# Performance work log

Hardware: AMD Instinct MI355X
Metric: run time of the kernel (lower is better)

Reference implementation:

```python
import jax, jax.numpy as jnp
import numpy as np

# Module config (mirrors SWTLayer(__init__) with dimensions=[64,64,16], kmax=[3,3], wavelet='db1')
DIMS = (64, 64)      # spatial sizes along axes 1,2
LEVELS = (6, 6)      # pywt.dwt_max_level(64, dec_len=2) == 6 (Haar)
KMAX = (3, 3)
NLIFT = 16
BATCH = 32


def swt_haar(x, level, axis):
    """pywt.swt(x, 'db1', level, trim_approx=True, norm=True) along `axis` (periodic).
    norm=True Haar level-j step s=2^(j-1): cA[i]=(a[i]+a[i+s])/2, cD[i]=(a[i]-a[i+s])/2.
    Returns concat([cA_n, cD_n, ..., cD_1]) along axis (length (level+1)*M)."""
    a = x
    details = []
    for j in range(level):
        s = 2 ** j
        sh = jnp.roll(a, -s, axis)   # a[i + s] (periodic)
        details.append((a - sh) * 0.5)
        a = (a + sh) * 0.5
    return jnp.concatenate([a] + details[::-1], axis=axis)


def iswt_haar(xt, level, axis):
    """pywt.iswt inverse of swt_haar: averages the two phase reconstructions per level."""
    bands = jnp.split(xt, level + 1, axis=axis)  # [cA_n, cD_n, ..., cD_1]
    a = bands[0]
    for j in range(level, 0, -1):
        cD = bands[level - j + 1]
        s = 2 ** (j - 1)
        a = 0.5 * ((a + cD) + jnp.roll(a - cD, s, axis))
    return a


def setup_inputs() -> dict:
    key = jax.random.key(0)
    k1, k2, k3 = jax.random.split(key, 3)
    x = jax.random.normal(k1, (BATCH, DIMS[0], DIMS[1], NLIFT), dtype=jnp.float32)
    W = jax.random.uniform(
        k2,
        (NLIFT, NLIFT, DIMS[0] * (LEVELS[0] + 1), DIMS[1] * (LEVELS[1] + 1)),
        dtype=jnp.float32,
    )
    b = jax.random.normal(k3, (NLIFT, NLIFT), dtype=jnp.float32)
    return {"x": x, "weights": W, "bias": b}


def reference(x, weights, bias):
    # forward SWT along each spatial axis -> (B, 448, 448, C)
    xt = x
    for i, L in enumerate(LEVELS):
        xt = swt_haar(xt, L, axis=i + 1)
    # truncate: zero wavenumber bands [kmax*M, level*M) along each spatial axis
    for i, (M, L, K) in enumerate(zip(DIMS, LEVELS, KMAX)):
        idx = (slice(None),) * (i + 1) + (slice(K * M, L * M),)
        xt = xt.at[idx].set(0.0)
    # per-location channel mixing: 'abcd,debc->abce'
    xt = jnp.einsum('abcd,debc->abce', xt, weights)
    # inverse SWT back to (B, 64, 64, C)
    out = xt
    for i, L in enumerate(LEVELS):
        out = iswt_haar(out, L, axis=i + 1)
    # skip path: F.linear(x, bias) == x @ bias.T
    return out + x @ bias.T
```

## Files before the change

### kernel.cpp

```cpp
#include <hip/hip_runtime.h>
#include <cstddef>
#include <cstdint>


#define X1_IDX(a,u,j,d) ((((size_t)(a)*256 + (u))*64 + (j))*16 + (d))

__global__ __launch_bounds__(256, 2) void k_swt1(const float* __restrict__ x,
                                                 float* __restrict__ X1) {
  __shared__ float col[64 * 64];
  __shared__ float Ps[4][64];
  const int t = threadIdx.x;
  const int q = t >> 6, c = t & 63, jl = c >> 4, d = c & 15;
  const int a = blockIdx.x, j = blockIdx.y * 4 + jl;
  const float* xp = x + ((size_t)a * 4096 + j) * 16 + d + (size_t)(q * 16) * 1024;
  float P = 0.f;
#pragma unroll
  for (int r = 0; r < 16; ++r) {
    float v = xp[(size_t)r * 1024];
    col[(q * 16 + r) * 64 + c] = v;
    P += v;
  }
  Ps[q][c] = P;
  __syncthreads();
  const float cA = (Ps[0][c] + Ps[1][c] + Ps[2][c] + Ps[3][c]) * 0.015625f;
  float w4 = Ps[q][c], w4b = Ps[(q + 1) & 3][c];
  float w5 = w4 + w4b;
  float* X1p = X1 + X1_IDX(a, 0, j, d);
#pragma unroll
  for (int r = 0; r < 16; ++r) {
    const int u = q * 16 + r;
    const float c0 = col[u * 64 + c];
    const float c1 = col[((u + 1) & 63) * 64 + c];
    const float c16 = col[((u + 16) & 63) * 64 + c];
    const float c32 = col[((u + 32) & 63) * 64 + c];
    X1p[(size_t)(u) * 1024]       = cA;
    X1p[(size_t)(64 + u) * 1024]  = w5 * 0.03125f - cA;
    X1p[(size_t)(128 + u) * 1024] = (w4 - w4b) * 0.03125f;
    X1p[(size_t)(192 + u) * 1024] = (c0 - c1) * 0.5f;
    w4 += c16 - c0;
    w4b += c32 - c16;
    w5 += c32 - c0;
  }
}

#define TSS 20
#define TSA (256 * TSS)
#define TS2(a,v,d) ((a) * TSA + (v) * TSS + (d))
#define WLS 18

__global__ __launch_bounds__(256, 2) void k_fused(float* __restrict__ X1,
                                                  const float* __restrict__ W) {
  __shared__ float Ts[2 * TSA];
  __shared__ float Wl[2 * 256 * WLS];
  __shared__ float Ps[2 * 8 * 16];
  const int t = threadIdx.x;
  const int bid = blockIdx.x;
  const int u = (bid & 7) + 8 * (bid >> 7);
  const int ac = (bid >> 3) & 15;
  const int a0 = ac * 2;
  const int ub = u >> 6;
  const int Brow = (ub == 3 ? 6 : ub) * 64 + (u & 63);

  const int aA = t >> 7, qA = (t >> 4) & 7, dA = t & 15;

  {
    const float* xp = X1 + X1_IDX(a0 + aA, u, qA * 8, dA);
    float P = 0.f;
#pragma unroll
    for (int r = 0; r < 8; ++r) {
      float v = xp[r * 16];
      Ts[TS2(aA, 192 + qA * 8 + r, dA)] = v;
      P += v;
    }
    Ps[aA * 128 + qA * 16 + dA] = P;
  }
  __syncthreads();
  {
    float cA = 0.f;
#pragma unroll
    for (int k = 0; k < 8; ++k) cA += Ps[aA * 128 + k * 16 + dA];
    cA *= 0.015625f;
    float w4 = Ps[aA * 128 + qA * 16 + dA] + Ps[aA * 128 + (((qA + 1) & 7) * 16) + dA];
    float w4b = Ps[aA * 128 + (((qA + 2) & 7) * 16) + dA] + Ps[aA * 128 + (((qA + 3) & 7) * 16) + dA];
    float w5 = w4 + w4b;
    float cd1[8];
#pragma unroll
    for (int r = 0; r < 8; ++r) {
      const int v = qA * 8 + r;
      const float c0 = Ts[TS2(aA, 192 + v, dA)];
      const float c1 = Ts[TS2(aA, 192 + ((v + 1) & 63), dA)];
      const float c16 = Ts[TS2(aA, 192 + ((v + 16) & 63), dA)];
      const float c32 = Ts[TS2(aA, 192 + ((v + 32) & 63), dA)];
      Ts[TS2(aA, v, dA)]       = cA;
      Ts[TS2(aA, 64 + v, dA)]  = w5 * 0.03125f - cA;
      Ts[TS2(aA, 128 + v, dA)] = (w4 - w4b) * 0.03125f;
      cd1[r] = (c0 - c1) * 0.5f;
      w4 += c16 - c0;
      w4b += c32 - c16;
      w5 += c32 - c0;
    }
    __syncthreads();
#pragma unroll
    for (int r = 0; r < 8; ++r) Ts[TS2(aA, 192 + qA * 8 + r, dA)] = cd1[r];
  }
  __syncthreads();

  const int vl = t >> 4, e = t & 15;
  const float* wbase = W + (size_t)t * 200704 + (size_t)Brow * 448;
  float4 pw0, pw1, pw2, pw3;
  {
    const float* wp = wbase;
    pw0 = *(const float4*)(wp + 0);
    pw1 = *(const float4*)(wp + 4);
    pw2 = *(const float4*)(wp + 8);
    pw3 = *(const float4*)(wp + 12);
  }
  for (int vg = 0; vg < 16; ++vg) {
    const int buf = vg & 1;
    {
      float* wrow = &Wl[(buf * 256 + t) * WLS];
      *(float2*)&wrow[0]  = make_float2(pw0.x, pw0.y);
      *(float2*)&wrow[2]  = make_float2(pw0.z, pw0.w);
      *(float2*)&wrow[4]  = make_float2(pw1.x, pw1.y);
      *(float2*)&wrow[6]  = make_float2(pw1.z, pw1.w);
      *(float2*)&wrow[8]  = make_float2(pw2.x, pw2.y);
      *(float2*)&wrow[10] = make_float2(pw2.z, pw2.w);
      *(float2*)&wrow[12] = make_float2(pw3.x, pw3.y);
      *(float2*)&wrow[14] = make_float2(pw3.z, pw3.w);
    }
    __syncthreads();
    if (vg < 15) {
      const int v2 = vg + 1;
      const int kb2 = v2 >> 2;
      const float* wp = wbase + (kb2 == 3 ? 384 : kb2 * 64) + (v2 & 3) * 16;
      pw0 = *(const float4*)(wp + 0);
      pw1 = *(const float4*)(wp + 4);
      pw2 = *(const float4*)(wp + 8);
      pw3 = *(const float4*)(wp + 12);
    }
    float wreg[16];
#pragma unroll
    for (int d = 0; d < 16; ++d)
      wreg[d] = Wl[(buf * 256 + d * 16 + e) * WLS + vl];
    const int v = vg * 16 + vl;
#pragma unroll
    for (int a = 0; a < 2; ++a) {
      const float4 t0 = *(const float4*)&Ts[TS2(a, v, 0)];
      const float4 t1 = *(const float4*)&Ts[TS2(a, v, 4)];
      const float4 t2 = *(const float4*)&Ts[TS2(a, v, 8)];
      const float4 t3 = *(const float4*)&Ts[TS2(a, v, 12)];
      float acc = t0.x * wreg[0] + t0.y * wreg[1] + t0.z * wreg[2] + t0.w * wreg[3]
                + t1.x * wreg[4] + t1.y * wreg[5] + t1.z * wreg[6] + t1.w * wreg[7]
                + t2.x * wreg[8] + t2.y * wreg[9] + t2.z * wreg[10] + t2.w * wreg[11]
                + t3.x * wreg[12] + t3.y * wreg[13] + t3.z * wreg[14] + t3.w * wreg[15];
      Ts[TS2(a, v, e)] = acc;
    }
  }
  __syncthreads();

  {
    const int aC = t >> 7, qC = (t >> 4) & 7, eC = t & 15;
    float rg[8];
#pragma unroll
    for (int r = 0; r < 8; ++r) {
      const int i = qC * 8 + r, i2 = (i - 32) & 63;
      rg[r] = 0.5f * (Ts[TS2(aC, i, eC)] + Ts[TS2(aC, 64 + i, eC)]
                    + Ts[TS2(aC, i2, eC)] - Ts[TS2(aC, 64 + i2, eC)]);
    }
    __syncthreads();
#pragma unroll
    for (int r = 0; r < 8; ++r) Ts[TS2(aC, qC * 8 + r, eC)] = rg[r];
    __syncthreads();
#pragma unroll
    for (int r = 0; r < 8; ++r) {
      const int i = qC * 8 + r, i2 = (i - 16) & 63;
      rg[r] = 0.5f * (Ts[TS2(aC, i, eC)] + Ts[TS2(aC, 128 + i, eC)]
                    + Ts[TS2(aC, i2, eC)] - Ts[TS2(aC, 128 + i2, eC)]);
    }
    __syncthreads();
#pragma unroll
    for (int r = 0; r < 8; ++r) Ts[TS2(aC, 64 + qC * 8 + r, eC)] = rg[r];
    __syncthreads();
#pragma unroll
    for (int r = 0; r < 8; ++r) {
      const int i = qC * 8 + r;
      float s = 0.f;
#pragma unroll
      for (int k = 0; k < 8; ++k) s += Ts[TS2(aC, 64 + ((i - 2 * k) & 63), eC)];
      rg[r] = s * 0.125f;
    }
    __syncthreads();
#pragma unroll
    for (int r = 0; r < 8; ++r) Ts[TS2(aC, qC * 8 + r, eC)] = rg[r];
    __syncthreads();
    float* zp = X1 + X1_IDX(a0 + aC, u, 0, eC);
#pragma unroll
    for (int r = 0; r < 8; ++r) {
      const int i = qC * 8 + r, i2 = (i - 1) & 63;
      zp[i * 16] = 0.5f * (Ts[TS2(aC, i, eC)] + Ts[TS2(aC, 192 + i, eC)]
                         + Ts[TS2(aC, i2, eC)] - Ts[TS2(aC, 192 + i2, eC)]);
    }
  }
}

__global__ __launch_bounds__(256, 2) void k_iswt1(const float* __restrict__ Z1,
                                                  const float* __restrict__ x,
                                                  const float* __restrict__ bias,
                                                  float* __restrict__ out) {
  __shared__ float A[64 * 64], Bb[64 * 64], D[64 * 64], xs[64 * 64];
  const int t = threadIdx.x;
  const int q = t >> 6, c = t & 63, jl = c >> 4, e = c & 15;
  const int a = blockIdx.x, j = blockIdx.y * 4 + jl;
  float breg[16];
  {
    const float4 b0 = *(const float4*)&bias[e * 16 + 0];
    const float4 b1 = *(const float4*)&bias[e * 16 + 4];
    const float4 b2 = *(const float4*)&bias[e * 16 + 8];
    const float4 b3 = *(const float4*)&bias[e * 16 + 12];
    breg[0]=b0.x; breg[1]=b0.y; breg[2]=b0.z; breg[3]=b0.w;
    breg[4]=b1.x; breg[5]=b1.y; breg[6]=b1.z; breg[7]=b1.w;
    breg[8]=b2.x; breg[9]=b2.y; breg[10]=b2.z; breg[11]=b2.w;
    breg[12]=b3.x; breg[13]=b3.y; breg[14]=b3.z; breg[15]=b3.w;
  }
  const float* Zp = Z1 + (size_t)a * 262144 + (size_t)j * 16 + e;
#pragma unroll
  for (int r = 0; r < 16; ++r) {
    const int i = q * 16 + r;
    A[i * 64 + c] = Zp[(size_t)i * 1024];
    D[i * 64 + c] = Zp[(size_t)(64 + i) * 1024];
    xs[i * 64 + c] = x[((size_t)a * 4096 + (size_t)i * 64 + j) * 16 + e];
  }
  __syncthreads();
  float rg[16];
#pragma unroll
  for (int r = 0; r < 16; ++r) {
    const int i = q * 16 + r, i2 = (i - 32) & 63;
    rg[r] = 0.5f * (A[i * 64 + c] + D[i * 64 + c] + A[i2 * 64 + c] - D[i2 * 64 + c]);
  }
  __syncthreads();
#pragma unroll
  for (int r = 0; r < 16; ++r) {
    const int i = q * 16 + r;
    Bb[i * 64 + c] = rg[r];
    D[i * 64 + c] = Zp[(size_t)(128 + i) * 1024];
  }
  __syncthreads();
#pragma unroll
  for (int r = 0; r < 16; ++r) {
    const int i = q * 16 + r, i2 = (i - 16) & 63;
    rg[r] = 0.5f * (Bb[i * 64 + c] + D[i * 64 + c] + Bb[i2 * 64 + c] - D[i2 * 64 + c]);
  }
  __syncthreads();
#pragma unroll
  for (int r = 0; r < 16; ++r) {
    const int i = q * 16 + r;
    A[i * 64 + c] = rg[r];
    D[i * 64 + c] = Zp[(size_t)(192 + i) * 1024];
  }
  __syncthreads();
#pragma unroll
  for (int r = 0; r < 16; ++r) {
    const int i = q * 16 + r;
    float s = 0.f;
#pragma unroll
    for (int k = 0; k < 8; ++k) s += A[((i - 2 * k) & 63) * 64 + c];
    rg[r] = s * 0.125f;
  }
  __syncthreads();
#pragma unroll
  for (int r = 0; r < 16; ++r) Bb[(q * 16 + r) * 64 + c] = rg[r];
  __syncthreads();
#pragma unroll
  for (int r = 0; r < 16; ++r) {
    const int i = q * 16 + r, i2 = (i - 1) & 63;
    float v = 0.5f * (Bb[i * 64 + c] + D[i * 64 + c] + Bb[i2 * 64 + c] - D[i2 * 64 + c]);
    float s = 0.f;
#pragma unroll
    for (int dd = 0; dd < 16; ++dd) s += xs[i * 64 + jl * 16 + dd] * breg[dd];
    out[((size_t)a * 4096 + (size_t)i * 64 + j) * 16 + e] = v + s;
  }
}

extern "C" void kernel_launch(void* const* d_in, const int* in_sizes, int n_in,
                              void* d_out, int out_size, void* d_ws, size_t ws_size,
                              hipStream_t stream) {
  const float* x = (const float*)d_in[0];
  const float* W = (const float*)d_in[1];
  const float* bias = (const float*)d_in[2];
  float* out = (float*)d_out;
  float* X1 = (float*)d_ws;

  k_swt1<<<dim3(32, 16), 256, 0, stream>>>(x, X1);
  k_fused<<<dim3(4096), 256, 0, stream>>>(X1, W);
  k_iswt1<<<dim3(32, 16), 256, 0, stream>>>(X1, x, bias, out);
}
```

Measured before the change: 421.0 us.

## Batch eight samples per fused block with dedicated weight-loader threads and register tiling

The fused kernel now handles 8 batch samples per block (512 threads, 1024 blocks), so each weight tile fetched from global memory is reused across 8 samples instead of 2. One wavefront acts as a dedicated weight loader that prefetches the next tile while 128 compute threads each calculate a 4x4 sample-by-output-channel register tile. The forward SWT kernel is vectorized to float4 over channels, the 8-tap running sum in both inverse stages becomes a sliding-window update, and the bias skip path uses float4 shared loads. Only a quarter of the threads do the einsum, and the larger shared footprint limits occupancy, which may cost latency hiding.

```diff
diff --git a/kernel.cpp b/kernel.cpp
--- a/kernel.cpp
+++ b/kernel.cpp
@@ -7,198 +7,264 @@
 
 __global__ __launch_bounds__(256, 2) void k_swt1(const float* __restrict__ x,
                                                  float* __restrict__ X1) {
-  __shared__ float col[64 * 64];
-  __shared__ float Ps[4][64];
+  __shared__ float col[64 * 256];
+  __shared__ float Ps[4 * 256];
   const int t = threadIdx.x;
-  const int q = t >> 6, c = t & 63, jl = c >> 4, d = c & 15;
-  const int a = blockIdx.x, j = blockIdx.y * 4 + jl;
-  const float* xp = x + ((size_t)a * 4096 + j) * 16 + d + (size_t)(q * 16) * 1024;
-  float P = 0.f;
-#pragma unroll
-  for (int r = 0; r < 16; ++r) {
-    float v = xp[(size_t)r * 1024];
-    col[(q * 16 + r) * 64 + c] = v;
-    P += v;
-  }
-  Ps[q][c] = P;
-  __syncthreads();
-  const float cA = (Ps[0][c] + Ps[1][c] + Ps[2][c] + Ps[3][c]) * 0.015625f;
-  float w4 = Ps[q][c], w4b = Ps[(q + 1) & 3][c];
-  float w5 = w4 + w4b;
-  float* X1p = X1 + X1_IDX(a, 0, j, d);
+  const int q = t >> 6;
+  const int cc = (t & 63) * 4;
+  const int jl = (t & 63) >> 2, dq = t & 3;
+  const int a = blockIdx.x, j = blockIdx.y * 16 + jl;
+  const float4* xp4 = (const float4*)(x + ((size_t)a * 4096 + j) * 16 + dq * 4);
+  float4 P = make_float4(0.f, 0.f, 0.f, 0.f);
+#pragma unroll
+  for (int r = 0; r < 16; ++r) {
+    const int i = q * 16 + r;
+    float4 v = xp4[(size_t)i * 256];
+    *(float4*)&col[i * 256 + cc] = v;
+    P.x += v.x; P.y += v.y; P.z += v.z; P.w += v.w;
+  }
+  *(float4*)&Ps[q * 256 + cc] = P;
+  __syncthreads();
+  const float4 p0 = *(const float4*)&Ps[0 * 256 + cc];
+  const float4 p1 = *(const float4*)&Ps[1 * 256 + cc];
+  const float4 p2 = *(const float4*)&Ps[2 * 256 + cc];
+  const float4 p3 = *(const float4*)&Ps[3 * 256 + cc];
+  float4 cA;
+  cA.x = (p0.x + p1.x + p2.x + p3.x) * 0.015625f;
+  cA.y = (p0.y + p1.y + p2.y + p3.y) * 0.015625f;
+  cA.z = (p0.z + p1.z + p2.z + p3.z) * 0.015625f;
+  cA.w = (p0.w + p1.w + p2.w + p3.w) * 0.015625f;
+  float4 w4 = *(const float4*)&Ps[q * 256 + cc];
+  float4 w4b = *(const float4*)&Ps[((q + 1) & 3) * 256 + cc];
+  float4 w5;
+  w5.x = w4.x + w4b.x; w5.y = w4.y + w4b.y; w5.z = w4.z + w4b.z; w5.w = w4.w + w4b.w;
+  float4* X1p = (float4*)(X1 + X1_IDX(a, 0, j, dq * 4));
+  float4 c0 = *(const float4*)&col[(q * 16) * 256 + cc];
 #pragma unroll
   for (int r = 0; r < 16; ++r) {
     const int u = q * 16 + r;
-    const float c0 = col[u * 64 + c];
-    const float c1 = col[((u + 1) & 63) * 64 + c];
-    const float c16 = col[((u + 16) & 63) * 64 + c];
-    const float c32 = col[((u + 32) & 63) * 64 + c];
-    X1p[(size_t)(u) * 1024]       = cA;
-    X1p[(size_t)(64 + u) * 1024]  = w5 * 0.03125f - cA;
-    X1p[(size_t)(128 + u) * 1024] = (w4 - w4b) * 0.03125f;
-    X1p[(size_t)(192 + u) * 1024] = (c0 - c1) * 0.5f;
-    w4 += c16 - c0;
-    w4b += c32 - c16;
-    w5 += c32 - c0;
+    const float4 c1 = *(const float4*)&col[((u + 1) & 63) * 256 + cc];
+    const float4 c16 = *(const float4*)&col[((u + 16) & 63) * 256 + cc];
+    const float4 c32 = *(const float4*)&col[((u + 32) & 63) * 256 + cc];
+    float4 b1, b2v, b3;
+    b1.x = w5.x * 0.03125f - cA.x; b1.y = w5.y * 0.03125f - cA.y;
+    b1.z = w5.z * 0.03125f - cA.z; b1.w = w5.w * 0.03125f - cA.w;
+    b2v.x = (w4.x - w4b.x) * 0.03125f; b2v.y = (w4.y - w4b.y) * 0.03125f;
+    b2v.z = (w4.z - w4b.z) * 0.03125f; b2v.w = (w4.w - w4b.w) * 0.03125f;
+    b3.x = (c0.x - c1.x) * 0.5f; b3.y = (c0.y - c1.y) * 0.5f;
+    b3.z = (c0.z - c1.z) * 0.5f; b3.w = (c0.w - c1.w) * 0.5f;
+    X1p[(size_t)u * 256] = cA;
+    X1p[(size_t)(64 + u) * 256] = b1;
+    X1p[(size_t)(128 + u) * 256] = b2v;
+    X1p[(size_t)(192 + u) * 256] = b3;
+    w4.x += c16.x - c0.x; w4.y += c16.y - c0.y; w4.z += c16.z - c0.z; w4.w += c16.w - c0.w;
+    w4b.x += c32.x - c16.x; w4b.y += c32.y - c16.y; w4b.z += c32.z - c16.z; w4b.w += c32.w - c16.w;
+    w5.x += c32.x - c0.x; w5.y += c32.y - c0.y; w5.z += c32.z - c0.z; w5.w += c32.w - c0.w;
+    c0 = c1;
   }
 }
 
-#define TSS 20
-#define TSA (256 * TSS)
-#define TS2(a,v,d) ((a) * TSA + (v) * TSS + (d))
-#define WLS 18
-
-__global__ __launch_bounds__(256, 2) void k_fused(float* __restrict__ X1,
+#define TSA 4104
+#define TS(a,v,d) ((a) * TSA + (v) * 16 + (d))
+#define WLS_E 324
+#define WLS_V 20
+
+__global__ __launch_bounds__(512, 1) void k_fused(float* __restrict__ X1,
                                                   const float* __restrict__ W) {
-  __shared__ float Ts[2 * TSA];
-  __shared__ float Wl[2 * 256 * WLS];
-  __shared__ float Ps[2 * 8 * 16];
+  __shared__ float Ts[8 * TSA];
+  __shared__ float Wl[16 * WLS_E];
+  __shared__ float Ps[8 * 4 * 16];
   const int t = threadIdx.x;
   const int bid = blockIdx.x;
-  const int u = (bid & 7) + 8 * (bid >> 7);
-  const int ac = (bid >> 3) & 15;
-  const int a0 = ac * 2;
+  const int u = (bid & 7) * 32 + (bid >> 5);
+  const int ac = (bid >> 3) & 3;
+  const int a0 = ac * 8;
   const int ub = u >> 6;
   const int Brow = (ub == 3 ? 6 : ub) * 64 + (u & 63);
 
-  const int aA = t >> 7, qA = (t >> 4) & 7, dA = t & 15;
+  const bool isLoader = (t >= 128 && t < 192);
+  const int ldq = (t >> 4) & 3, lel = t & 15;
+  float pw[4][16];
+
+  if (isLoader) {
+#pragma unroll
+    for (int jd = 0; jd < 4; ++jd) {
+      const int d = ldq * 4 + jd;
+      const float* wp = W + (size_t)(d * 16 + lel) * 200704 + (size_t)Brow * 448;
+#pragma unroll
+      for (int vq = 0; vq < 4; ++vq) {
+        float4 v = *(const float4*)(wp + vq * 4);
+        pw[jd][vq * 4 + 0] = v.x; pw[jd][vq * 4 + 1] = v.y;
+        pw[jd][vq * 4 + 2] = v.z; pw[jd][vq * 4 + 3] = v.w;
+      }
+    }
+  }
 
   {
-    const float* xp = X1 + X1_IDX(a0 + aA, u, qA * 8, dA);
+    const int aA = t >> 6, qA = (t >> 4) & 3, dA = t & 15;
+    const float* xpA = X1 + X1_IDX(a0 + aA, u, qA * 16, dA);
     float P = 0.f;
 #pragma unroll
-    for (int r = 0; r < 8; ++r) {
-      float v = xp[r * 16];
-      Ts[TS2(aA, 192 + qA * 8 + r, dA)] = v;
+    for (int r = 0; r < 16; ++r) {
+      float v = xpA[r * 16];
+      Ts[TS(aA, 192 + qA * 16 + r, dA)] = v;
       P += v;
     }
-    Ps[aA * 128 + qA * 16 + dA] = P;
-  }
-  __syncthreads();
+    Ps[(aA * 4 + qA) * 16 + dA] = P;
+    __syncthreads();
+    const float S = Ps[(aA * 4 + 0) * 16 + dA] + Ps[(aA * 4 + 1) * 16 + dA]
+                  + Ps[(aA * 4 + 2) * 16 + dA] + Ps[(aA * 4 + 3) * 16 + dA];
+    const float cA = S * 0.015625f;
+    float w4 = Ps[(aA * 4 + qA) * 16 + dA];
+    float w4b = Ps[(aA * 4 + ((qA + 1) & 3)) * 16 + dA];
+    float w5 = w4 + w4b;
+    float cd1[16];
+    float c0 = Ts[TS(aA, 192 + qA * 16, dA)];
+#pragma unroll
+    for (int r = 0; r < 16; ++r) {
+      const int v = qA * 16 + r;
+      const float c1 = Ts[TS(aA, 192 + ((v + 1) & 63), dA)];
+      const float c16 = Ts[TS(aA, 192 + ((v + 16) & 63), dA)];
+      const float c32 = Ts[TS(aA, 192 + ((v + 32) & 63), dA)];
+      Ts[TS(aA, v, dA)] = cA;
+      Ts[TS(aA, 64 + v, dA)] = w5 * 0.03125f - cA;
+      Ts[TS(aA, 128 + v, dA)] = (w4 - w4b) * 0.03125f;
+      cd1[r] = (c0 - c1) * 0.5f;
+      w4 += c16 - c0; w4b += c32 - c16; w5 += c32 - c0;
+      c0 = c1;
+    }
+    __syncthreads();
+#pragma unroll
+    for (int r = 0; r < 16; ++r) Ts[TS(aA, 192 + qA * 16 + r, dA)] = cd1[r];
+  }
+  __syncthreads();
+  if (isLoader) {
+#pragma unroll
+    for (int vl = 0; vl < 16; ++vl) {
+      float4 o = make_float4(pw[0][vl], pw[1][vl], pw[2][vl], pw[3][vl]);
+      *(float4*)&Wl[lel * WLS_E + vl * WLS_V + ldq * 4] = o;
+    }
+  }
+  __syncthreads();
+
   {
-    float cA = 0.f;
-#pragma unroll
-    for (int k = 0; k < 8; ++k) cA += Ps[aA * 128 + k * 16 + dA];
-    cA *= 0.015625f;
-    float w4 = Ps[aA * 128 + qA * 16 + dA] + Ps[aA * 128 + (((qA + 1) & 7) * 16) + dA];
-    float w4b = Ps[aA * 128 + (((qA + 2) & 7) * 16) + dA] + Ps[aA * 128 + (((qA + 3) & 7) * 16) + dA];
-    float w5 = w4 + w4b;
-    float cd1[8];
-#pragma unroll
-    for (int r = 0; r < 8; ++r) {
-      const int v = qA * 8 + r;
-      const float c0 = Ts[TS2(aA, 192 + v, dA)];
-      const float c1 = Ts[TS2(aA, 192 + ((v + 1) & 63), dA)];
-      const float c16 = Ts[TS2(aA, 192 + ((v + 16) & 63), dA)];
-      const float c32 = Ts[TS2(aA, 192 + ((v + 32) & 63), dA)];
-      Ts[TS2(aA, v, dA)]       = cA;
-      Ts[TS2(aA, 64 + v, dA)]  = w5 * 0.03125f - cA;
-      Ts[TS2(aA, 128 + v, dA)] = (w4 - w4b) * 0.03125f;
-      cd1[r] = (c0 - c1) * 0.5f;
-      w4 += c16 - c0;
-      w4b += c32 - c16;
-      w5 += c32 - c0;
-    }
-    __syncthreads();
-#pragma unroll
-    for (int r = 0; r < 8; ++r) Ts[TS2(aA, 192 + qA * 8 + r, dA)] = cd1[r];
-  }
-  __syncthreads();
-
-  const int vl = t >> 4, e = t & 15;
-  const float* wbase = W + (size_t)t * 200704 + (size_t)Brow * 448;
-  float4 pw0, pw1, pw2, pw3;
+    const bool isCompute = (t < 128);
+    const int at = t >> 6, et = (t >> 4) & 3, vlB = t & 15;
+    for (int vg = 0; vg < 16; ++vg) {
+      float4 tf[4][4], wf[4][4];
+      float acc[4][4];
+      if (isCompute) {
+        const int v = vg * 16 + vlB;
+#pragma unroll
+        for (int ja = 0; ja < 4; ++ja)
+#pragma unroll
+          for (int dq = 0; dq < 4; ++dq)
+            tf[ja][dq] = *(const float4*)&Ts[TS(at * 4 + ja, v, dq * 4)];
+#pragma unroll
+        for (int je = 0; je < 4; ++je)
+#pragma unroll
+          for (int dq = 0; dq < 4; ++dq)
+            wf[je][dq] = *(const float4*)&Wl[(et * 4 + je) * WLS_E + vlB * WLS_V + dq * 4];
+      }
+      if (isLoader && vg < 15) {
+        const int v2 = vg + 1, kb = v2 >> 2;
+        const int Ccol = (kb == 3 ? 6 : kb) * 64 + (v2 & 3) * 16;
+#pragma unroll
+        for (int jd = 0; jd < 4; ++jd) {
+          const int d = ldq * 4 + jd;
+          const float* wp = W + (size_t)(d * 16 + lel) * 200704 + (size_t)Brow * 448 + Ccol;
+#pragma unroll
+          for (int vq = 0; vq < 4; ++vq) {
+            float4 v = *(const float4*)(wp + vq * 4);
+            pw[jd][vq * 4 + 0] = v.x; pw[jd][vq * 4 + 1] = v.y;
+            pw[jd][vq * 4 + 2] = v.z; pw[jd][vq * 4 + 3] = v.w;
+          }
+        }
+      }
+      if (isCompute) {
+#pragma unroll
+        for (int ja = 0; ja < 4; ++ja)
+#pragma unroll
+          for (int je = 0; je < 4; ++je) {
+            float s = 0.f;
+#pragma unroll
+            for (int dq = 0; dq < 4; ++dq) {
+              s += tf[ja][dq].x * wf[je][dq].x;
+              s += tf[ja][dq].y * wf[je][dq].y;
+              s += tf[ja][dq].z * wf[je][dq].z;
+              s += tf[ja][dq].w * wf[je][dq].w;
+            }
+            acc[ja][je] = s;
+          }
+      }
+      __syncthreads();
+      if (isCompute) {
+        const int v = vg * 16 + vlB;
+#pragma unroll
+        for (int ja = 0; ja < 4; ++ja) {
+          float4 o = make_float4(acc[ja][0], acc[ja][1], acc[ja][2], acc[ja][3]);
+          *(float4*)&Ts[TS(at * 4 + ja, v, et * 4)] = o;
+        }
+      }
+      if (isLoader && vg < 15) {
+#pragma unroll
+        for (int vl = 0; vl < 16; ++vl) {
+          float4 o = make_float4(pw[0][vl], pw[1][vl], pw[2][vl], pw[3][vl]);
+          *(float4*)&Wl[lel * WLS_E + vl * WLS_V + ldq * 4] = o;
+        }
+      }
+      __syncthreads();
+    }
+  }
+
   {
-    const float* wp = wbase;
-    pw0 = *(const float4*)(wp + 0);
-    pw1 = *(const float4*)(wp + 4);
-    pw2 = *(const float4*)(wp + 8);
-    pw3 = *(const float4*)(wp + 12);
-  }
-  for (int vg = 0; vg < 16; ++vg) {
-    const int buf = vg & 1;
+    const int aC = t >> 6, qC = (t >> 4) & 3, eC = t & 15;
+    float rg[16];
+#pragma unroll
+    for (int r = 0; r < 16; ++r) {
+      const int i = qC * 16 + r, i2 = (i - 32) & 63;
+      rg[r] = 0.5f * (Ts[TS(aC, i, eC)] + Ts[TS(aC, 64 + i, eC)]
+                    + Ts[TS(aC, i2, eC)] - Ts[TS(aC, 64 + i2, eC)]);
+    }
+    __syncthreads();
+#pragma unroll
+    for (int r = 0; r < 16; ++r) Ts[TS(aC, qC * 16 + r, eC)] = rg[r];
+    __syncthreads();
+#pragma unroll
+    for (int r = 0; r < 16; ++r) {
+      const int i = qC * 16 + r, i2 = (i - 16) & 63;
+      rg[r] = 0.5f * (Ts[TS(aC, i, eC)] + Ts[TS(aC, 128 + i, eC)]
+                    + Ts[TS(aC, i2, eC)] - Ts[TS(aC, 128 + i2, eC)]);
+    }
+    __syncthreads();
+#pragma unroll
+    for (int r = 0; r < 16; ++r) Ts[TS(aC, 64 + qC * 16 + r, eC)] = rg[r];
+    __syncthreads();
     {
-      float* wrow = &Wl[(buf * 256 + t) * WLS];
-      *(float2*)&wrow[0]  = make_float2(pw0.x, pw0.y);
-      *(float2*)&wrow[2]  = make_float2(pw0.z, pw0.w);
-      *(float2*)&wrow[4]  = make_float2(pw1.x, pw1.y);
-      *(float2*)&wrow[6]  = make_float2(pw1.z, pw1.w);
-      *(float2*)&wrow[8]  = make_float2(pw2.x, pw2.y);
-      *(float2*)&wrow[10] = make_float2(pw2.z, pw2.w);
-      *(float2*)&wrow[12] = make_float2(pw3.x, pw3.y);
-      *(float2*)&wrow[14] = make_float2(pw3.z, pw3.w);
-    }
-    __syncthreads();
-    if (vg < 15) {
-      const int v2 = vg + 1;
-      const int kb2 = v2 >> 2;
-      const float* wp = wbase + (kb2 == 3 ? 384 : kb2 * 64) + (v2 & 3) * 16;
-      pw0 = *(const float4*)(wp + 0);
-      pw1 = *(const float4*)(wp + 4);
-      pw2 = *(const float4*)(wp + 8);
-      pw3 = *(const float4*)(wp + 12);
-    }
-    float wreg[16];
-#pragma unroll
-    for (int d = 0; d < 16; ++d)
-      wreg[d] = Wl[(buf * 256 + d * 16 + e) * WLS + vl];
-    const int v = vg * 16 + vl;
-#pragma unroll
-    for (int a = 0; a < 2; ++a) {
-      const float4 t0 = *(const float4*)&Ts[TS2(a, v, 0)];
-      const float4 t1 = *(const float4*)&Ts[TS2(a, v, 4)];
-      const float4 t2 = *(const float4*)&Ts[TS2(a, v, 8)];
-      const float4 t3 = *(const float4*)&Ts[TS2(a, v, 12)];
-      float acc = t0.x * wreg[0] + t0.y * wreg[1] + t0.z * wreg[2] + t0.w * wreg[3]
-                + t1.x * wreg[4] + t1.y * wreg[5] + t1.z * wreg[6] + t1.w * wreg[7]
-                + t2.x * wreg[8] + t2.y * wreg[9] + t2.z * wreg[10] + t2.w * wreg[11]
-                + t3.x * wreg[12] + t3.y * wreg[13] + t3.z * wreg[14] + t3.w * wreg[15];
-      Ts[TS2(a, v, e)] = acc;
-    }
-  }
-  __syncthreads();
-
-  {
-    const int aC = t >> 7, qC = (t >> 4) & 7, eC = t & 15;
-    float rg[8];
-#pragma unroll
-    for (int r = 0; r < 8; ++r) {
-      const int i = qC * 8 + r, i2 = (i - 32) & 63;
-      rg[r] = 0.5f * (Ts[TS2(aC, i, eC)] + Ts[TS2(aC, 64 + i, eC)]
-                    + Ts[TS2(aC, i2, eC)] - Ts[TS2(aC, 64 + i2, eC)]);
-    }
-    __syncthreads();
-#pragma unroll
-    for (int r = 0; r < 8; ++r) Ts[TS2(aC, qC * 8 + r, eC)] = rg[r];
-    __syncthreads();
-#pragma unroll
-    for (int r = 0; r < 8; ++r) {
-      const int i = qC * 8 + r, i2 = (i - 16) & 63;
-      rg[r] = 0.5f * (Ts[TS2(aC, i, eC)] + Ts[TS2(aC, 128 + i, eC)]
-                    + Ts[TS2(aC, i2, eC)] - Ts[TS2(aC, 128 + i2, eC)]);
-    }
-    __syncthreads();
-#pragma unroll
-    for (int r = 0; r < 8; ++r) Ts[TS2(aC, 64 + qC * 8 + r, eC)] = rg[r];
-    __syncthreads();
-#pragma unroll
-    for (int r = 0; r < 8; ++r) {
-      const int i = qC * 8 + r;
-      float s = 0.f;
-#pragma unroll
-      for (int k = 0; k < 8; ++k) s += Ts[TS2(aC, 64 + ((i - 2 * k) & 63), eC)];
-      rg[r] = s * 0.125f;
-    }
-    __syncthreads();
-#pragma unroll
-    for (int r = 0; r < 8; ++r) Ts[TS2(aC, qC * 8 + r, eC)] = rg[r];
+      float s0 = 0.f, s1 = 0.f;
+#pragma unroll
+      for (int k = 0; k < 8; ++k) s0 += Ts[TS(aC, 64 + ((qC * 16 - 2 * k) & 63), eC)];
+#pragma unroll
+      for (int k = 0; k < 8; ++k) s1 += Ts[TS(aC, 64 + ((qC * 16 + 1 - 2 * k) & 63), eC)];
+      rg[0] = s0 * 0.125f; rg[1] = s1 * 0.125f;
+#pragma unroll
+      for (int r = 2; r < 16; ++r) {
+        const int i = qC * 16 + r;
+        const float add = Ts[TS(aC, 64 + i, eC)] - Ts[TS(aC, 64 + ((i - 16) & 63), eC)];
+        if (r & 1) { s1 += add; rg[r] = s1 * 0.125f; }
+        else       { s0 += add; rg[r] = s0 * 0.125f; }
+      }
+    }
+    __syncthreads();
+#pragma unroll
+    for (int r = 0; r < 16; ++r) Ts[TS(aC, qC * 16 + r, eC)] = rg[r];
     __syncthreads();
     float* zp = X1 + X1_IDX(a0 + aC, u, 0, eC);
 #pragma unroll
-    for (int r = 0; r < 8; ++r) {
-      const int i = qC * 8 + r, i2 = (i - 1) & 63;
-      zp[i * 16] = 0.5f * (Ts[TS2(aC, i, eC)] + Ts[TS2(aC, 192 + i, eC)]
-                         + Ts[TS2(aC, i2, eC)] - Ts[TS2(aC, 192 + i2, eC)]);
+    for (int r = 0; r < 16; ++r) {
+      const int i = qC * 16 + r, i2 = (i - 1) & 63;
+      zp[i * 16] = 0.5f * (Ts[TS(aC, i, eC)] + Ts[TS(aC, 192 + i, eC)]
+                         + Ts[TS(aC, i2, eC)] - Ts[TS(aC, 192 + i2, eC)]);
     }
   }
 }
@@ -211,17 +277,9 @@
   const int t = threadIdx.x;
   const int q = t >> 6, c = t & 63, jl = c >> 4, e = c & 15;
   const int a = blockIdx.x, j = blockIdx.y * 4 + jl;
-  float breg[16];
-  {
-    const float4 b0 = *(const float4*)&bias[e * 16 + 0];
-    const float4 b1 = *(const float4*)&bias[e * 16 + 4];
-    const float4 b2 = *(const float4*)&bias[e * 16 + 8];
-    const float4 b3 = *(const float4*)&bias[e * 16 + 12];
-    breg[0]=b0.x; breg[1]=b0.y; breg[2]=b0.z; breg[3]=b0.w;
-    breg[4]=b1.x; breg[5]=b1.y; breg[6]=b1.z; breg[7]=b1.w;
-    breg[8]=b2.x; breg[9]=b2.y; breg[10]=b2.z; breg[11]=b2.w;
-    breg[12]=b3.x; breg[13]=b3.y; breg[14]=b3.z; breg[15]=b3.w;
-  }
+  float4 bregs[4];
+#pragma unroll
+  for (int dq = 0; dq < 4; ++dq) bregs[dq] = *(const float4*)&bias[e * 16 + dq * 4];
   const float* Zp = Z1 + (size_t)a * 262144 + (size_t)j * 16 + e;
 #pragma unroll
   for (int r = 0; r < 16; ++r) {
@@ -258,13 +316,20 @@
     D[i * 64 + c] = Zp[(size_t)(192 + i) * 1024];
   }
   __syncthreads();
-#pragma unroll
-  for (int r = 0; r < 16; ++r) {
-    const int i = q * 16 + r;
-    float s = 0.f;
-#pragma unroll
-    for (int k = 0; k < 8; ++k) s += A[((i - 2 * k) & 63) * 64 + c];
-    rg[r] = s * 0.125f;
+  {
+    float s0 = 0.f, s1 = 0.f;
+#pragma unroll
+    for (int k = 0; k < 8; ++k) s0 += A[(((q * 16) - 2 * k) & 63) * 64 + c];
+#pragma unroll
+    for (int k = 0; k < 8; ++k) s1 += A[(((q * 16 + 1) - 2 * k) & 63) * 64 + c];
+    rg[0] = s0 * 0.125f; rg[1] = s1 * 0.125f;
+#pragma unroll
+    for (int r = 2; r < 16; ++r) {
+      const int i = q * 16 + r;
+      const float add = A[i * 64 + c] - A[((i - 16) & 63) * 64 + c];
+      if (r & 1) { s1 += add; rg[r] = s1 * 0.125f; }
+      else       { s0 += add; rg[r] = s0 * 0.125f; }
+    }
   }
   __syncthreads();
 #pragma unroll
@@ -273,10 +338,15 @@
 #pragma unroll
   for (int r = 0; r < 16; ++r) {
     const int i = q * 16 + r, i2 = (i - 1) & 63;
-    float v = 0.5f * (Bb[i * 64 + c] + D[i * 64 + c] + Bb[i2 * 64 + c] - D[i2 * 64 + c]);
-    float s = 0.f;
-#pragma unroll
-    for (int dd = 0; dd < 16; ++dd) s += xs[i * 64 + jl * 16 + dd] * breg[dd];
+    const float v = 0.5f * (Bb[i * 64 + c] + D[i * 64 + c] + Bb[i2 * 64 + c] - D[i2 * 64 + c]);
+    const float4 x0 = *(const float4*)&xs[i * 64 + jl * 16 + 0];
+    const float4 x1 = *(const float4*)&xs[i * 64 + jl * 16 + 4];
+    const float4 x2 = *(const float4*)&xs[i * 64 + jl * 16 + 8];
+    const float4 x3 = *(const float4*)&xs[i * 64 + jl * 16 + 12];
+    float s = x0.x * bregs[0].x + x0.y * bregs[0].y + x0.z * bregs[0].z + x0.w * bregs[0].w
+            + x1.x * bregs[1].x + x1.y * bregs[1].y + x1.z * bregs[1].z + x1.w * bregs[1].w
+            + x2.x * bregs[2].x + x2.y * bregs[2].y + x2.z * bregs[2].z + x2.w * bregs[2].w
+            + x3.x * bregs[3].x + x3.y * bregs[3].y + x3.z * bregs[3].z + x3.w * bregs[3].w;
     out[((size_t)a * 4096 + (size_t)i * 64 + j) * 16 + e] = v + s;
   }
 }
@@ -290,7 +360,7 @@
   float* out = (float*)d_out;
   float* X1 = (float*)d_ws;
 
-  k_swt1<<<dim3(32, 16), 256, 0, stream>>>(x, X1);
-  k_fused<<<dim3(4096), 256, 0, stream>>>(X1, W);
+  k_swt1<<<dim3(32, 4), 256, 0, stream>>>(x, X1);
+  k_fused<<<dim3(1024), 512, 0, stream>>>(X1, W);
   k_iswt1<<<dim3(32, 16), 256, 0, stream>>>(X1, x, bias, out);
 }
```

Result: slower. 645.9 us (+53.4%).
